# Kernel tuning notes

Measured on AMD Instinct MI355X. Metric: run time of the kernel, lower is better.

The kernel has to match this reference:

```python
import jax, jax.numpy as jnp
import numpy as np

H = 1024      # hidden_size
I = 4096      # intermediate_size
E = 8         # num_experts
TOP_K = 2
LB_COEF = 0.01


def setup_inputs() -> dict:
    key = jax.random.key(0)
    ks = jax.random.split(key, 8)
    s_h = 1.0 / np.sqrt(H)
    s_i = 1.0 / np.sqrt(I)
    return {
        "x": jax.random.normal(ks[0], (2, 2048, H), dtype=jnp.float32),
        "Wr": jax.random.normal(ks[1], (H, E), dtype=jnp.float32) * s_h,
        "br": jnp.zeros((E,), dtype=jnp.float32),
        "W1": jax.random.normal(ks[2], (E, H, I), dtype=jnp.float32) * s_h,
        "b1": jnp.zeros((E, I), dtype=jnp.float32),
        "W2": jax.random.normal(ks[3], (E, I, H), dtype=jnp.float32) * s_i,
        "b2": jnp.zeros((E, H), dtype=jnp.float32),
    }


def _moe_forward(x, Wr, br, W1, b1, W2, b2):
    B, S, Hd = x.shape
    x_flat = x.reshape(-1, Hd)                      # [T, H]
    T = x_flat.shape[0]

    # ---- Router: softmax probs, top-k, renormalize ----
    logits = x_flat @ Wr + br                       # [T, E]
    probs = jax.nn.softmax(logits, axis=-1)         # [T, E]
    topk_w, topk_idx = jax.lax.top_k(probs, TOP_K)  # [T, K]
    topk_w = topk_w / jnp.sum(topk_w, axis=-1, keepdims=True)

    # ---- Load-balance aux loss (switch-style) ----
    onehot = jax.nn.one_hot(topk_idx, E, dtype=x.dtype)   # [T, K, E]
    frac_tokens = onehot.mean(axis=(0, 1))                 # [E]
    frac_probs = probs.mean(axis=0)                        # [E]
    aux_loss = E * jnp.sum(frac_tokens * frac_probs) * LB_COEF

    # combine_weights[t, e] = routing weight of expert e for token t (0 if unselected)
    combine = jnp.sum(topk_w[..., None] * onehot, axis=1)  # [T, E]

    # ---- Experts: dense per-expert FFN, weighted combine ----
    out = jnp.zeros_like(x_flat)
    for e in range(E):
        h = jax.nn.gelu(x_flat @ W1[e] + b1[e])            # [T, I]
        y = h @ W2[e] + b2[e]                              # [T, H]
        out = out + y * combine[:, e:e + 1]
    return out.reshape(B, S, Hd), aux_loss


def reference(x, Wr, br, W1, b1, W2, b2):
    return _moe_forward(x, Wr, br, W1, b1, W2, b2)
```

## Files before the change

### kernel.cpp

```cpp
#include <hip/hip_runtime.h>
#include <hip/hip_bf16.h>

#define HD 1024
#define ID 4096
#define NE 8
#define NT 4096
#define NSLOT (NT*2)

typedef __attribute__((ext_vector_type(4))) float f32x4;
typedef __attribute__((ext_vector_type(8))) short bf16x8;
typedef __attribute__((ext_vector_type(4))) unsigned int u32x4;
typedef __attribute__((ext_vector_type(2))) unsigned int u32x2;
typedef unsigned short u16;

__device__ __forceinline__ u16 f2b(float f) {
  __hip_bfloat16 h = __float2bfloat16(f);
  return __builtin_bit_cast(unsigned short, h);
}
__device__ __forceinline__ unsigned int pack2(float a, float b) {
  return (unsigned int)f2b(a) | ((unsigned int)f2b(b) << 16);
}
__device__ __forceinline__ void gload16(const void* g, void* l) {
  __builtin_amdgcn_global_load_lds(
      (const __attribute__((address_space(1))) unsigned int*)g,
      (__attribute__((address_space(3))) unsigned int*)l, 16, 0, 0);
}
__device__ __forceinline__ float gelu_tanh(float v) {
  float c = v + 0.044715f * v * v * v;
  return 0.5f * v * (1.0f + tanhf(0.7978845608028654f * c));
}

__global__ void k_convert_x(const float* __restrict__ x, u16* __restrict__ xb) {
  int i = blockIdx.x * 256 + threadIdx.x;
  const f32x4* x4 = (const f32x4*)x;
  f32x4 a = x4[2 * i], b = x4[2 * i + 1];
  u32x4 r;
  r[0] = pack2(a[0], a[1]); r[1] = pack2(a[2], a[3]);
  r[2] = pack2(b[0], b[1]); r[3] = pack2(b[2], b[3]);
  ((u32x4*)xb)[i] = r;
}

__global__ __launch_bounds__(256) void k_transpose_bf16(
    const float* __restrict__ src, u16* __restrict__ dst, int R, int C) {
  __shared__ float tile[64][65];
  int e = blockIdx.z;
  int c0 = blockIdx.x * 64;
  int r0 = blockIdx.y * 64;
  int t = threadIdx.x;
  const float* s = src + (size_t)e * R * C;
#pragma unroll
  for (int i = 0; i < 16; ++i) {
    int r = i * 4 + (t >> 6);
    tile[r][t & 63] = s[(size_t)(r0 + r) * C + c0 + (t & 63)];
  }
  __syncthreads();
  u16* d = dst + (size_t)e * R * C;
#pragma unroll
  for (int i = 0; i < 4; ++i) {
    int c = i * 16 + (t >> 4);
    int rb = (t & 15) * 4;
    u32x2 p;
    p[0] = pack2(tile[rb + 0][c], tile[rb + 1][c]);
    p[1] = pack2(tile[rb + 2][c], tile[rb + 3][c]);
    *(u32x2*)&d[(size_t)(c0 + c) * R + r0 + rb] = p;
  }
}

__global__ __launch_bounds__(256) void k_router(
    const float* __restrict__ x, const float* __restrict__ Wr,
    const float* __restrict__ br, int* __restrict__ cnt,
    int* __restrict__ slotE, int* __restrict__ slotLoc,
    float* __restrict__ slotW, float* __restrict__ probsAll) {
  __shared__ float wrt[NE * HD];
  int t = threadIdx.x;
  for (int i = t; i < NE * HD; i += 256) wrt[(i & 7) * HD + (i >> 3)] = Wr[i];
  __syncthreads();
  int wave = t >> 6, lane = t & 63;
  int token = blockIdx.x * 4 + wave;
  const float* xr = x + (size_t)token * HD;
  float acc[NE] = {0, 0, 0, 0, 0, 0, 0, 0};
#pragma unroll 4
  for (int j = 0; j < 16; ++j) {
    int h = j * 64 + lane;
    float xv = xr[h];
#pragma unroll
    for (int e = 0; e < NE; ++e) acc[e] += xv * wrt[e * HD + h];
  }
#pragma unroll
  for (int d = 1; d < 64; d <<= 1) {
#pragma unroll
    for (int e = 0; e < NE; ++e) acc[e] += __shfl_xor(acc[e], d, 64);
  }
  if (lane == 0) {
    float lg[NE], p[NE];
    float m = -1e30f;
#pragma unroll
    for (int e = 0; e < NE; ++e) { lg[e] = acc[e] + br[e]; m = fmaxf(m, lg[e]); }
    float s = 0.f;
#pragma unroll
    for (int e = 0; e < NE; ++e) { p[e] = expf(lg[e] - m); s += p[e]; }
    float inv = 1.0f / s;
    int i1 = 0, i2 = -1;
    float v1 = -1.f, v2 = -1.f;
#pragma unroll
    for (int e = 0; e < NE; ++e) {
      p[e] *= inv;
      probsAll[token * NE + e] = p[e];
      if (p[e] > v1) { v2 = v1; i2 = i1; v1 = p[e]; i1 = e; }
      else if (p[e] > v2) { v2 = p[e]; i2 = e; }
    }
    float wsum = v1 + v2;
    int l1 = atomicAdd(&cnt[i1], 1);
    int l2 = atomicAdd(&cnt[i2], 1);
    slotE[token * 2] = i1;     slotLoc[token * 2] = l1;     slotW[token * 2] = v1 / wsum;
    slotE[token * 2 + 1] = i2; slotLoc[token * 2 + 1] = l2; slotW[token * 2 + 1] = v2 / wsum;
  }
}

__global__ __launch_bounds__(256) void k_psum(const float* __restrict__ probsAll,
                                              float* __restrict__ psumG) {
  __shared__ float red[256];
  int t = threadIdx.x;
  int base = blockIdx.x * 128;
  float s = 0.f;
  for (int i = t >> 3; i < 128; i += 32) s += probsAll[(base + i) * NE + (t & 7)];
  red[t] = s;
  __syncthreads();
  for (int st = 128; st >= 8; st >>= 1) {
    if (t < st) red[t] += red[t + st];
    __syncthreads();
  }
  if (t < 8) atomicAdd(&psumG[t], red[t]);
}

__global__ void k_finalize(const float* __restrict__ psumG, const int* __restrict__ cnt,
                           int* __restrict__ off, float* __restrict__ out_aux) {
  if (threadIdx.x == 0) {
    int o = 0;
    float a = 0.f;
    for (int e = 0; e < NE; ++e) {
      off[e] = o;
      o += cnt[e];
      a += ((float)cnt[e] / (float)NSLOT) * (psumG[e] / (float)NT);
    }
    off[NE] = o;
    out_aux[0] = (float)NE * a * 0.01f;
  }
}

__global__ void k_scatter(const int* __restrict__ slotE, const int* __restrict__ slotLoc,
                          const float* __restrict__ slotW, const int* __restrict__ off,
                          int* __restrict__ rowTok, float* __restrict__ rowW) {
  int i = blockIdx.x * 256 + threadIdx.x;
  int pos = off[slotE[i]] + slotLoc[i];
  if (pos < 0) pos = 0;
  if (pos >= NSLOT) pos = NSLOT - 1;
  rowTok[pos] = i >> 1;
  rowW[pos] = slotW[i];
}

#define STG(bf) do { \
    gload16(srcA0, &As[bf][c0 * 8]); \
    gload16(srcA1, &As[bf][c1 * 8]); \
    gload16(srcB0, &Bs[bf][c0 * 8]); \
    gload16(srcB1, &Bs[bf][c1 * 8]); \
    srcA0 += 32; srcA1 += 32; srcB0 += 32; srcB1 += 32; \
  } while (0)

__global__ __launch_bounds__(256, 3) void k_gemm1(
    const u16* __restrict__ xb, const u16* __restrict__ w1t,
    const float* __restrict__ b1, u16* __restrict__ hbuf,
    const int* __restrict__ cnt, const int* __restrict__ off,
    const int* __restrict__ rowTok) {
  const int NWG = NE * 32 * 32;
  int bid = blockIdx.x;
  int wg = (bid & 7) * (NWG / 8) + (bid >> 3);
  int e = wg >> 10;
  int rem = wg & 1023;
  int m0 = (rem >> 5) * 128;
  int n0 = (rem & 31) * 128;
  int ce = cnt[e];
  if (m0 >= ce) return;
  int oe = off[e];
  __shared__ u16 As[3][128 * 32];
  __shared__ u16 Bs[3][128 * 32];
  __shared__ int rtok[128];
  int t = threadIdx.x;
  if (t < 128) {
    int r = m0 + t;
    if (r >= ce) r = ce - 1;
    int tok = rowTok[oe + r];
    rtok[t] = (tok < 0) ? 0 : (tok >= NT ? NT - 1 : tok);
  }
  __syncthreads();
  int c0 = t, c1 = t + 256;
  int js0 = (c0 & 3) ^ ((c0 >> 3) & 3);
  int js1 = (c1 & 3) ^ ((c1 >> 3) & 3);
  const u16* srcA0 = xb + (size_t)rtok[c0 >> 2] * HD + js0 * 8;
  const u16* srcA1 = xb + (size_t)rtok[c1 >> 2] * HD + js1 * 8;
  const u16* bb = w1t + (size_t)e * ID * HD + (size_t)n0 * HD;
  const u16* srcB0 = bb + (size_t)(c0 >> 2) * HD + js0 * 8;
  const u16* srcB1 = bb + (size_t)(c1 >> 2) * HD + js1 * 8;
  int wave = t >> 6, lane = t & 63;
  int wr = wave >> 1, wc = wave & 1;
  int arow = wr * 64 + (lane & 15);
  int aoff = arow * 32 + ((lane >> 4) ^ ((arow >> 1) & 3)) * 8;
  int brow = wc * 64 + (lane & 15);
  int boff = brow * 32 + ((lane >> 4) ^ ((brow >> 1) & 3)) * 8;
  f32x4 acc[4][4] = {};
  const int NK = HD / 32;
  STG(0);
  STG(1);
  int rb = 0;
  for (int kt = 0; kt < NK; ++kt) {
    if (kt + 1 < NK) asm volatile("s_waitcnt vmcnt(4)" ::: "memory");
    else             asm volatile("s_waitcnt vmcnt(0)" ::: "memory");
    __builtin_amdgcn_s_barrier();
    const u16* ap = &As[rb][aoff];
    const u16* bp = &Bs[rb][boff];
    bf16x8 af[4], bfr[4];
#pragma unroll
    for (int m = 0; m < 4; ++m) af[m] = *(const bf16x8*)(ap + m * 16 * 32);
#pragma unroll
    for (int n = 0; n < 4; ++n) bfr[n] = *(const bf16x8*)(bp + n * 16 * 32);
#pragma unroll
    for (int m = 0; m < 4; ++m)
#pragma unroll
      for (int n = 0; n < 4; ++n)
        acc[m][n] = __builtin_amdgcn_mfma_f32_16x16x32_bf16(af[m], bfr[n], acc[m][n], 0, 0, 0);
    if (kt + 2 < NK) {
      int sb = rb + 2; if (sb >= 3) sb -= 3;
      STG(sb);
    }
    rb = (rb == 2) ? 0 : rb + 1;
  }
  const float* b1e = b1 + (size_t)e * ID + n0;
#pragma unroll
  for (int n = 0; n < 4; ++n) {
    int col = wc * 64 + n * 16 + (lane & 15);
    float bias = b1e[col];
#pragma unroll
    for (int m = 0; m < 4; ++m) {
      int rbase = wr * 64 + m * 16 + (lane >> 4) * 4;
#pragma unroll
      for (int r = 0; r < 4; ++r) {
        int grow = m0 + rbase + r;
        if (grow < ce) {
          float v = acc[m][n][r] + bias;
          hbuf[(size_t)(oe + grow) * ID + n0 + col] = f2b(gelu_tanh(v));
        }
      }
    }
  }
}

__global__ __launch_bounds__(256, 3) void k_gemm2(
    const u16* __restrict__ hbuf, const u16* __restrict__ w2t,
    const float* __restrict__ b2, float* __restrict__ out,
    const int* __restrict__ cnt, const int* __restrict__ off,
    const int* __restrict__ rowTok, const float* __restrict__ rowW) {
  const int NWG = NE * 32 * 2 * 8;
  int bid = blockIdx.x;
  int wg = (bid & 7) * (NWG / 8) + (bid >> 3);
  int e = wg >> 9;
  int rem = wg & 511;
  int m0 = (rem >> 4) * 128;
  int ks = (rem >> 3) & 1;
  int n0 = (rem & 7) * 128;
  int ce = cnt[e];
  if (m0 >= ce) return;
  int oe = off[e];
  int k0 = ks * (ID / 2);
  __shared__ u16 As[3][128 * 32];
  __shared__ u16 Bs[3][128 * 32];
  __shared__ int rtok[128];
  __shared__ float rw[128];
  int t = threadIdx.x;
  if (t < 128) {
    int r = m0 + t;
    int rc = (r < ce) ? r : ce - 1;
    int tok = rowTok[oe + rc];
    rtok[t] = (tok < 0) ? 0 : (tok >= NT ? NT - 1 : tok);
    rw[t] = (r < ce) ? rowW[oe + r] : 0.0f;
  }
  __syncthreads();
  int c0 = t, c1 = t + 256;
  int js0 = (c0 & 3) ^ ((c0 >> 3) & 3);
  int js1 = (c1 & 3) ^ ((c1 >> 3) & 3);
  int rA0 = m0 + (c0 >> 2); if (rA0 >= ce) rA0 = ce - 1;
  int rA1 = m0 + (c1 >> 2); if (rA1 >= ce) rA1 = ce - 1;
  const u16* srcA0 = hbuf + (size_t)(oe + rA0) * ID + k0 + js0 * 8;
  const u16* srcA1 = hbuf + (size_t)(oe + rA1) * ID + k0 + js1 * 8;
  const u16* bb = w2t + (size_t)e * HD * ID + (size_t)n0 * ID + k0;
  const u16* srcB0 = bb + (size_t)(c0 >> 2) * ID + js0 * 8;
  const u16* srcB1 = bb + (size_t)(c1 >> 2) * ID + js1 * 8;
  int wave = t >> 6, lane = t & 63;
  int wr = wave >> 1, wc = wave & 1;
  int arow = wr * 64 + (lane & 15);
  int aoff = arow * 32 + ((lane >> 4) ^ ((arow >> 1) & 3)) * 8;
  int brow = wc * 64 + (lane & 15);
  int boff = brow * 32 + ((lane >> 4) ^ ((brow >> 1) & 3)) * 8;
  f32x4 acc[4][4] = {};
  const int NK = (ID / 2) / 32;
  STG(0);
  STG(1);
  int rb = 0;
  for (int kt = 0; kt < NK; ++kt) {
    if (kt + 1 < NK) asm volatile("s_waitcnt vmcnt(4)" ::: "memory");
    else             asm volatile("s_waitcnt vmcnt(0)" ::: "memory");
    __builtin_amdgcn_s_barrier();
    const u16* ap = &As[rb][aoff];
    const u16* bp = &Bs[rb][boff];
    bf16x8 af[4], bfr[4];
#pragma unroll
    for (int m = 0; m < 4; ++m) af[m] = *(const bf16x8*)(ap + m * 16 * 32);
#pragma unroll
    for (int n = 0; n < 4; ++n) bfr[n] = *(const bf16x8*)(bp + n * 16 * 32);
#pragma unroll
    for (int m = 0; m < 4; ++m)
#pragma unroll
      for (int n = 0; n < 4; ++n)
        acc[m][n] = __builtin_amdgcn_mfma_f32_16x16x32_bf16(af[m], bfr[n], acc[m][n], 0, 0, 0);
    if (kt + 2 < NK) {
      int sb = rb + 2; if (sb >= 3) sb -= 3;
      STG(sb);
    }
    rb = (rb == 2) ? 0 : rb + 1;
  }
  const float* b2e = b2 + (size_t)e * HD + n0;
#pragma unroll
  for (int n = 0; n < 4; ++n) {
    int col = wc * 64 + n * 16 + (lane & 15);
    float bias = (ks == 0) ? b2e[col] : 0.0f;
#pragma unroll
    for (int m = 0; m < 4; ++m) {
      int rbase = wr * 64 + m * 16 + (lane >> 4) * 4;
#pragma unroll
      for (int r = 0; r < 4; ++r) {
        int grow = m0 + rbase + r;
        if (grow < ce) {
          float v = (acc[m][n][r] + bias) * rw[rbase + r];
          atomicAdd(&out[(size_t)rtok[rbase + r] * HD + n0 + col], v);
        }
      }
    }
  }
}

extern "C" void kernel_launch(void* const* d_in, const int* in_sizes, int n_in,
                              void* d_out, int out_size, void* d_ws, size_t ws_size,
                              hipStream_t stream) {
  const float* x  = (const float*)d_in[0];
  const float* Wr = (const float*)d_in[1];
  const float* br = (const float*)d_in[2];
  const float* W1 = (const float*)d_in[3];
  const float* b1 = (const float*)d_in[4];
  const float* W2 = (const float*)d_in[5];
  const float* b2 = (const float*)d_in[6];
  float* out = (float*)d_out;

  char* ws = (char*)d_ws;
  size_t o = 0;
  auto alloc = [&](size_t bytes) {
    void* p = ws + o;
    o = (o + bytes + 255) & ~(size_t)255;
    return p;
  };
  u16* xb    = (u16*)alloc((size_t)NT * HD * 2);
  u16* w1t   = (u16*)alloc((size_t)NE * ID * HD * 2);
  u16* w2t   = (u16*)alloc((size_t)NE * ID * HD * 2);
  u16* hbuf  = (u16*)alloc((size_t)NSLOT * ID * 2);
  int* cnt     = (int*)alloc(NE * 4);
  float* psumG = (float*)alloc(NE * 4);
  int* off     = (int*)alloc(16 * 4);
  int* slotE   = (int*)alloc(NSLOT * 4);
  int* slotLoc = (int*)alloc(NSLOT * 4);
  float* slotW = (float*)alloc(NSLOT * 4);
  int* rowTok  = (int*)alloc(NSLOT * 4);
  float* rowW  = (float*)alloc(NSLOT * 4);
  float* probsAll = (float*)alloc((size_t)NT * NE * 4);

  if (ws_size < o) return;

  hipMemsetAsync(cnt, 0, NE * 4, stream);
  hipMemsetAsync(psumG, 0, NE * 4, stream);
  hipMemsetAsync(out, 0, (size_t)out_size * 4, stream);
  k_convert_x<<<(NT * HD / 8) / 256, 256, 0, stream>>>(x, xb);
  k_transpose_bf16<<<dim3(ID / 64, HD / 64, NE), 256, 0, stream>>>(W1, w1t, HD, ID);
  k_transpose_bf16<<<dim3(HD / 64, ID / 64, NE), 256, 0, stream>>>(W2, w2t, ID, HD);
  k_router<<<NT / 4, 256, 0, stream>>>(x, Wr, br, cnt, slotE, slotLoc, slotW, probsAll);
  k_psum<<<32, 256, 0, stream>>>(probsAll, psumG);
  k_finalize<<<1, 64, 0, stream>>>(psumG, cnt, off, out + (size_t)NT * HD);
  k_scatter<<<NSLOT / 256, 256, 0, stream>>>(slotE, slotLoc, slotW, off, rowTok, rowW);
  k_gemm1<<<NE * 32 * 32, 256, 0, stream>>>(xb, w1t, b1, hbuf, cnt, off, rowTok);
  k_gemm2<<<NE * 32 * 2 * 8, 256, 0, stream>>>(hbuf, w2t, b2, out, cnt, off, rowTok, rowW);
}
```

Baseline: 499.4 us.

## Fuse x conversion and prob sums into router, merge transposes, reorder GEMM tiles

Folds the bf16 conversion of x and the per-expert probability sum into the router kernel, dropping the probsAll buffer, the k_convert_x kernel and the k_psum kernel. The two weight transposes become one launch. Both GEMMs change block-index decoding so M varies fastest, which groups blocks that share the same weight tile. GELU uses an exp-based tanh instead of tanhf. Shared-memory float atomics and the faster exp change rounding slightly.

New measurement: 519.6 us. 4.0% more time.

```diff
diff --git a/kernel.cpp b/kernel.cpp
--- a/kernel.cpp
+++ b/kernel.cpp
@@ -27,25 +27,30 @@
 }
 __device__ __forceinline__ float gelu_tanh(float v) {
   float c = v + 0.044715f * v * v * v;
-  return 0.5f * v * (1.0f + tanhf(0.7978845608028654f * c));
-}
-
-__global__ void k_convert_x(const float* __restrict__ x, u16* __restrict__ xb) {
-  int i = blockIdx.x * 256 + threadIdx.x;
-  const f32x4* x4 = (const f32x4*)x;
-  f32x4 a = x4[2 * i], b = x4[2 * i + 1];
-  u32x4 r;
-  r[0] = pack2(a[0], a[1]); r[1] = pack2(a[2], a[3]);
-  r[2] = pack2(b[0], b[1]); r[3] = pack2(b[2], b[3]);
-  ((u32x4*)xb)[i] = r;
-}
-
-__global__ __launch_bounds__(256) void k_transpose_bf16(
-    const float* __restrict__ src, u16* __restrict__ dst, int R, int C) {
+  float u = 1.5957691216057308f * c;
+  float t = 1.0f - 2.0f / (__expf(u) + 1.0f);
+  return 0.5f * v * (1.0f + t);
+}
+
+__global__ __launch_bounds__(256) void k_transpose2(
+    const float* __restrict__ W1, u16* __restrict__ w1t,
+    const float* __restrict__ W2, u16* __restrict__ w2t) {
   __shared__ float tile[64][65];
-  int e = blockIdx.z;
-  int c0 = blockIdx.x * 64;
-  int r0 = blockIdx.y * 64;
+  int id = blockIdx.x;
+  const float* src;
+  u16* dst;
+  int R, C, e, rem;
+  if (id < 8192) {
+    e = id >> 10; rem = id & 1023;
+    src = W1; dst = w1t; R = HD; C = ID;
+  } else {
+    id -= 8192;
+    e = id >> 10; rem = id & 1023;
+    src = W2; dst = w2t; R = ID; C = HD;
+  }
+  int ctiles = C >> 6;
+  int c0 = (rem % ctiles) * 64;
+  int r0 = (rem / ctiles) * 64;
   int t = threadIdx.x;
   const float* s = src + (size_t)e * R * C;
 #pragma unroll
@@ -70,19 +75,24 @@
     const float* __restrict__ x, const float* __restrict__ Wr,
     const float* __restrict__ br, int* __restrict__ cnt,
     int* __restrict__ slotE, int* __restrict__ slotLoc,
-    float* __restrict__ slotW, float* __restrict__ probsAll) {
+    float* __restrict__ slotW, float* __restrict__ psumG,
+    u16* __restrict__ xb) {
   __shared__ float wrt[NE * HD];
+  __shared__ float blkp[NE];
   int t = threadIdx.x;
+  if (t < NE) blkp[t] = 0.0f;
   for (int i = t; i < NE * HD; i += 256) wrt[(i & 7) * HD + (i >> 3)] = Wr[i];
   __syncthreads();
   int wave = t >> 6, lane = t & 63;
   int token = blockIdx.x * 4 + wave;
   const float* xr = x + (size_t)token * HD;
+  u16* xbr = xb + (size_t)token * HD;
   float acc[NE] = {0, 0, 0, 0, 0, 0, 0, 0};
 #pragma unroll 4
   for (int j = 0; j < 16; ++j) {
     int h = j * 64 + lane;
     float xv = xr[h];
+    xbr[h] = f2b(xv);
 #pragma unroll
     for (int e = 0; e < NE; ++e) acc[e] += xv * wrt[e * HD + h];
   }
@@ -105,7 +115,7 @@
 #pragma unroll
     for (int e = 0; e < NE; ++e) {
       p[e] *= inv;
-      probsAll[token * NE + e] = p[e];
+      atomicAdd(&blkp[e], p[e]);
       if (p[e] > v1) { v2 = v1; i2 = i1; v1 = p[e]; i1 = e; }
       else if (p[e] > v2) { v2 = p[e]; i2 = e; }
     }
@@ -115,22 +125,8 @@
     slotE[token * 2] = i1;     slotLoc[token * 2] = l1;     slotW[token * 2] = v1 / wsum;
     slotE[token * 2 + 1] = i2; slotLoc[token * 2 + 1] = l2; slotW[token * 2 + 1] = v2 / wsum;
   }
-}
-
-__global__ __launch_bounds__(256) void k_psum(const float* __restrict__ probsAll,
-                                              float* __restrict__ psumG) {
-  __shared__ float red[256];
-  int t = threadIdx.x;
-  int base = blockIdx.x * 128;
-  float s = 0.f;
-  for (int i = t >> 3; i < 128; i += 32) s += probsAll[(base + i) * NE + (t & 7)];
-  red[t] = s;
-  __syncthreads();
-  for (int st = 128; st >= 8; st >>= 1) {
-    if (t < st) red[t] += red[t + st];
-    __syncthreads();
-  }
-  if (t < 8) atomicAdd(&psumG[t], red[t]);
+  __syncthreads();
+  if (t < NE) atomicAdd(&psumG[t], blkp[t]);
 }
 
 __global__ void k_finalize(const float* __restrict__ psumG, const int* __restrict__ cnt,
@@ -177,8 +173,8 @@
   int wg = (bid & 7) * (NWG / 8) + (bid >> 3);
   int e = wg >> 10;
   int rem = wg & 1023;
-  int m0 = (rem >> 5) * 128;
-  int n0 = (rem & 31) * 128;
+  int n0 = (rem >> 5) * 128;
+  int m0 = (rem & 31) * 128;
   int ce = cnt[e];
   if (m0 >= ce) return;
   int oe = off[e];
@@ -264,9 +260,9 @@
   int wg = (bid & 7) * (NWG / 8) + (bid >> 3);
   int e = wg >> 9;
   int rem = wg & 511;
-  int m0 = (rem >> 4) * 128;
-  int ks = (rem >> 3) & 1;
-  int n0 = (rem & 7) * 128;
+  int ks = rem >> 8;
+  int n0 = ((rem >> 5) & 7) * 128;
+  int m0 = (rem & 31) * 128;
   int ce = cnt[e];
   if (m0 >= ce) return;
   int oe = off[e];
@@ -378,18 +374,14 @@
   float* slotW = (float*)alloc(NSLOT * 4);
   int* rowTok  = (int*)alloc(NSLOT * 4);
   float* rowW  = (float*)alloc(NSLOT * 4);
-  float* probsAll = (float*)alloc((size_t)NT * NE * 4);
 
   if (ws_size < o) return;
 
-  hipMemsetAsync(cnt, 0, NE * 4, stream);
-  hipMemsetAsync(psumG, 0, NE * 4, stream);
-  hipMemsetAsync(out, 0, (size_t)out_size * 4, stream);
-  k_convert_x<<<(NT * HD / 8) / 256, 256, 0, stream>>>(x, xb);
-  k_transpose_bf16<<<dim3(ID / 64, HD / 64, NE), 256, 0, stream>>>(W1, w1t, HD, ID);
-  k_transpose_bf16<<<dim3(HD / 64, ID / 64, NE), 256, 0, stream>>>(W2, w2t, ID, HD);
-  k_router<<<NT / 4, 256, 0, stream>>>(x, Wr, br, cnt, slotE, slotLoc, slotW, probsAll);
-  k_psum<<<32, 256, 0, stream>>>(probsAll, psumG);
+  (void)hipMemsetAsync(cnt, 0, NE * 4, stream);
+  (void)hipMemsetAsync(psumG, 0, NE * 4, stream);
+  (void)hipMemsetAsync(out, 0, (size_t)out_size * 4, stream);
+  k_transpose2<<<16384, 256, 0, stream>>>(W1, w1t, W2, w2t);
+  k_router<<<NT / 4, 256, 0, stream>>>(x, Wr, br, cnt, slotE, slotLoc, slotW, psumG, xb);
   k_finalize<<<1, 64, 0, stream>>>(psumG, cnt, off, out + (size_t)NT * HD);
   k_scatter<<<NSLOT / 256, 256, 0, stream>>>(slotE, slotLoc, slotW, off, rowTok, rowW);
   k_gemm1<<<NE * 32 * 32, 256, 0, stream>>>(xb, w1t, b1, hbuf, cnt, off, rowTok);
```
